# Kernel optimization log

Measured on AMD Instinct MI355X. Metric: run time of the kernel, lower is better.

## Reference

```python
import jax, jax.numpy as jnp
import numpy as np

GS, SO = 5, 3  # KANLinear grid_size, spline_order (efficient-kan defaults)


def kan_linear(x, base_w, spline_w, spline_scaler):
    """efficient-kan KANLinear: silu(x)@Wb^T + Bspline(x) contracted with scaled spline weights."""
    g = jnp.arange(-SO, GS + SO + 1, dtype=x.dtype) * (2.0 / GS) - 1.0  # uniform grid, len 12
    xe = x[..., None]                                                    # (..., in, 1)
    bases = ((xe >= g[:-1]) & (xe < g[1:])).astype(x.dtype)              # (..., in, 11)
    for k in range(1, SO + 1):  # Cox-de Boor recursion -> (..., in, 8)
        bases = ((xe - g[:-(k + 1)]) / (g[k:-1] - g[:-(k + 1)])) * bases[..., :-1] \
              + ((g[k + 1:] - xe) / (g[k + 1:] - g[1:-k])) * bases[..., 1:]
    out = jax.nn.silu(x) @ base_w.T
    return out + jnp.einsum('...ik,oik->...o', bases, spline_w * spline_scaler[..., None])


def reference(hidden_states, in_bw, in_sw, in_sc, conv_w, conv_b, x_bw, x_sw, x_sc,
              dt_w, dt_bias, A_logs, Ds, out_bw, out_sw, out_sc):
    B, N, L, Dm = hidden_states.shape
    d_inner, _, d_conv = conv_w.shape
    K = dt_bias.shape[0]          # 4 scan directions
    d_state = A_logs.shape[1]
    dt_rank = dt_w.shape[1]

    xz = kan_linear(hidden_states, in_bw, in_sw, in_sc)          # (B,N,L,2*Di)
    x, z = jnp.split(xz, 2, axis=-1)

    # causal depthwise conv1d + SiLU (torch pads both sides then truncates to L == left-pad)
    xc = x.reshape(B * N, L, d_inner).transpose(0, 2, 1)          # (BN,Di,L)
    xc = jax.lax.conv_general_dilated(xc, conv_w, (1,), [(d_conv - 1, 0)],
                                      dimension_numbers=('NCH', 'OIH', 'NCH'),
                                      feature_group_count=d_inner)
    xc = jax.nn.silu(xc + conv_b[None, :, None])
    x = xc.transpose(0, 2, 1).reshape(B, N, L, d_inner)

    xs = jnp.concatenate([x, jnp.flip(x, axis=2)], axis=1)        # (B,4,L,Di): fwd + seq-reversed

    x_dbl = kan_linear(xs, x_bw, x_sw, x_sc)                      # (B,4,L,R+2S)
    dt, Bs, Cs = jnp.split(x_dbl, [dt_rank, dt_rank + d_state], axis=-1)
    dts = dt @ dt_w.T                                             # (B,4,L,Di)
    delta = jax.nn.softplus(dts + dt_bias[None, :, None, :])      # (B,4,L,Di)
    A = -jnp.exp(A_logs).reshape(K, d_inner, d_state)             # (4,Di,S)

    # selective scan over L (serial data-dependent linear recurrence)
    u_t = xs.transpose(2, 0, 1, 3)      # (L,B,4,Di)
    d_t = delta.transpose(2, 0, 1, 3)   # (L,B,4,Di)
    B_t = Bs.transpose(2, 0, 1, 3)      # (L,B,4,S)
    C_t = Cs.transpose(2, 0, 1, 3)      # (L,B,4,S)

    def step(h, inp):
        u_l, dl, b_l, c_l = inp
        h = h * jnp.exp(dl[..., None] * A) + (dl * u_l)[..., None] * b_l[:, :, None, :]
        return h, jnp.einsum('bkdn,bkn->bkd', h, c_l)

    h0 = jnp.zeros((B, K, d_inner, d_state), xs.dtype)
    _, ys = jax.lax.scan(step, h0, (u_t, d_t, B_t, C_t))          # ys: (L,B,4,Di)

    y = ys.transpose(1, 2, 0, 3) + xs * Ds.reshape(K, d_inner)[None, :, None, :]  # (B,4,L,Di)
    y = y[:, :2] + jnp.flip(y[:, 2:4], axis=2)                    # merge forward/backward scans

    out = jnp.concatenate([y, z], axis=-1)                        # (B,2,L,2*Di)
    return kan_linear(out, out_bw, out_sw, out_sc)                # (B,2,L,Dm)


def setup_inputs() -> dict:
    key = jax.random.key(0)
    B, N, L = 2, 2, 1024
    d_model, d_state, d_conv, K = 512, 16, 4, 4
    d_inner = d_model            # expand=1
    dt_rank = 32                 # ceil(512/16)
    ks = jax.random.split(key, 10)

    def lin(k, o, i):
        return jax.random.normal(k, (o, i), jnp.float32) / np.sqrt(i).astype(np.float32)

    def spl(k, o, i):
        return jax.random.normal(k, (o, i, GS + SO), jnp.float32) * 0.05

    dt = jnp.exp(jax.random.uniform(ks[7], (d_inner,), jnp.float32)
                 * (np.log(0.1) - np.log(0.001)) + np.log(0.001))
    dt = jnp.clip(dt, 1e-4, None)
    inv_dt = dt + jnp.log(-jnp.expm1(-dt))

    std = dt_rank ** -0.5
    return {
        'hidden_states': jax.random.normal(ks[0], (B, N, L, d_model), jnp.float32),
        'in_bw': lin(ks[1], 2 * d_inner, d_model),
        'in_sw': spl(ks[2], 2 * d_inner, d_model),
        'in_sc': jnp.ones((2 * d_inner, d_model), jnp.float32),
        'conv_w': jax.random.normal(ks[3], (d_inner, 1, d_conv), jnp.float32) / np.sqrt(d_conv).astype(np.float32),
        'conv_b': jnp.zeros((d_inner,), jnp.float32),
        'x_bw': lin(ks[4], dt_rank + 2 * d_state, d_inner),
        'x_sw': spl(ks[5], dt_rank + 2 * d_state, d_inner),
        'x_sc': jnp.ones((dt_rank + 2 * d_state, d_inner), jnp.float32),
        'dt_w': jax.random.uniform(ks[6], (d_inner, dt_rank), jnp.float32, -std, std),
        'dt_bias': jnp.tile(inv_dt[None], (K, 1)),
        'A_logs': jnp.log(jnp.tile(jnp.arange(1, d_state + 1, dtype=jnp.float32)[None], (K * d_inner, 1))),
        'Ds': jnp.ones((K * d_inner,), jnp.float32),
        'out_bw': lin(ks[8], d_model, 2 * d_inner),
        'out_sw': spl(ks[9], d_model, 2 * d_inner),
        'out_sc': jnp.ones((d_model, 2 * d_inner), jnp.float32),
    }
```

## Files before the change

### kernel.cpp

```cpp
#include <hip/hip_runtime.h>
#include <stdint.h>

#define DEV __device__ __forceinline__

typedef __attribute__((ext_vector_type(8))) short short8;
typedef __attribute__((ext_vector_type(4))) float f32x4;

DEV unsigned short f2bf(float f) {
    union { float f; uint32_t u; } v; v.f = f;
    uint32_t u = v.u;
    return (unsigned short)((u + 0x7fffu + ((u >> 16) & 1u)) >> 16);
}
DEV float silu_f(float x) { return x / (1.0f + __expf(-x)); }

DEV void bspline8(float x, float* bo) {
    float b[11];
#pragma unroll
    for (int j = 0; j < 11; ++j) {
        float gj  = 0.4f * (float)(j - 3) - 1.0f;
        float gj1 = 0.4f * (float)(j - 2) - 1.0f;
        b[j] = (x >= gj && x < gj1) ? 1.0f : 0.0f;
    }
#pragma unroll
    for (int k = 1; k <= 3; ++k) {
        float inv = 1.0f / (0.4f * (float)k);
#pragma unroll
        for (int j = 0; j + k < 11; ++j) {
            float gj  = 0.4f * (float)(j - 3) - 1.0f;
            float gk1 = 0.4f * (float)(j + k - 2) - 1.0f;
            b[j] = ((x - gj) * b[j] + (gk1 - x) * b[j + 1]) * inv;
        }
    }
#pragma unroll
    for (int j = 0; j < 8; ++j) bo[j] = b[j];
}

__global__ __launch_bounds__(256) void zero_kernel(float4* __restrict__ p, int n4) {
    int i = blockIdx.x * 256 + threadIdx.x;
    if (i < n4) p[i] = make_float4(0.f, 0.f, 0.f, 0.f);
}

__global__ __launch_bounds__(256) void wc_kernel(const float* __restrict__ bw,
        const float* __restrict__ sw, const float* __restrict__ sc,
        unsigned short* __restrict__ Wc, int total) {
    int idx = blockIdx.x * 256 + threadIdx.x;
    if (idx >= total) return;
    float scale = sc[idx];
    unsigned short* o = Wc + (size_t)idx * 9;
    o[0] = f2bf(bw[idx]);
    const float* s = sw + (size_t)idx * 8;
#pragma unroll
    for (int j = 0; j < 8; ++j) o[1 + j] = f2bf(s[j] * scale);
}

__global__ __launch_bounds__(256) void feat_kernel(const float* __restrict__ X,
        unsigned short* __restrict__ F, int total) {
    int idx = blockIdx.x * 256 + threadIdx.x;
    if (idx >= total) return;
    float x = X[idx];
    unsigned short* o = F + (size_t)idx * 9;
    o[0] = f2bf(silu_f(x));
    float bo[8];
    bspline8(x, bo);
#pragma unroll
    for (int j = 0; j < 8; ++j) o[1 + j] = f2bf(bo[j]);
}

template<int BM, int BN, int DEPTH, bool ATOMIC>
__global__ __launch_bounds__(256) void gemm_mfma2(const unsigned short* __restrict__ A,
        const unsigned short* __restrict__ B, float* __restrict__ C,
        int M, int N, int K, int klen) {
    constexpr int NB  = DEPTH + 2;
    constexpr int FRM = BM / 32;
    constexpr int FRN = BN / 32;
    constexpr int GLA = (BM * 64) / 4096;
    constexpr int GLB = (BN * 64) / 4096;
    constexpr int GL  = GLA + GLB;
    constexpr int LDA = BM * 32;
    constexpr int LDB = BN * 32;
    __shared__ unsigned short As[NB * LDA];
    __shared__ unsigned short Bs[NB * LDB];

    const int tid = threadIdx.x;
    const int lane = tid & 63;
    const int w = tid >> 6;
    const int wr = w >> 1, wc = w & 1;
    const int bm = blockIdx.x * BM, bn = blockIdx.y * BN;
    const int kbase = blockIdx.z * klen;
    const int NT = klen / 32;
    const int frow = lane & 15;
    const int kq = (lane >> 4) * 8;

    f32x4 acc[FRM][FRN];
#pragma unroll
    for (int m = 0; m < FRM; ++m)
#pragma unroll
        for (int n = 0; n < FRN; ++n)
            acc[m][n] = (f32x4){0.f, 0.f, 0.f, 0.f};

    auto stage = [&](int t, int buf) {
        const int k0 = kbase + t * 32;
#pragma unroll
        for (int r = 0; r < GLA; ++r) {
            int bo = r * 4096 + tid * 16;
            int row = bo >> 6, cb = bo & 63;
            __builtin_amdgcn_global_load_lds(
                (const __attribute__((address_space(1))) void*)((const char*)A + ((size_t)(bm + row) * K + k0) * 2 + cb),
                (__attribute__((address_space(3))) void*)((char*)As + (size_t)buf * LDA * 2 + bo), 16, 0, 0);
        }
#pragma unroll
        for (int r = 0; r < GLB; ++r) {
            int bo = r * 4096 + tid * 16;
            int row = bo >> 6, cb = bo & 63;
            __builtin_amdgcn_global_load_lds(
                (const __attribute__((address_space(1))) void*)((const char*)B + ((size_t)(bn + row) * K + k0) * 2 + cb),
                (__attribute__((address_space(3))) void*)((char*)Bs + (size_t)buf * LDB * 2 + bo), 16, 0, 0);
        }
    };

    auto compute = [&](int buf) {
        const unsigned short* as = As + (size_t)buf * LDA;
        const unsigned short* bs = Bs + (size_t)buf * LDB;
        short8 af[FRM], bf[FRN];
#pragma unroll
        for (int m = 0; m < FRM; ++m)
            af[m] = *(const short8*)&as[(wr * (BM / 2) + m * 16 + frow) * 32 + kq];
#pragma unroll
        for (int n = 0; n < FRN; ++n)
            bf[n] = *(const short8*)&bs[(wc * (BN / 2) + n * 16 + frow) * 32 + kq];
#pragma unroll
        for (int m = 0; m < FRM; ++m)
#pragma unroll
            for (int n = 0; n < FRN; ++n)
                acc[m][n] = __builtin_amdgcn_mfma_f32_16x16x32_bf16(af[m], bf[n], acc[m][n], 0, 0, 0);
    };

    for (int t = 0; t < DEPTH; ++t) stage(t, t);

    int rb = 0;
    int sb = DEPTH;
    int t = 0;
    for (; t + DEPTH < NT; ++t) {
        stage(t + DEPTH, sb);
        asm volatile("s_waitcnt vmcnt(%0)" :: "i"(DEPTH * GL) : "memory");
        asm volatile("s_barrier" ::: "memory");
        compute(rb);
        rb = (rb + 1 == NB) ? 0 : rb + 1;
        sb = (sb + 1 == NB) ? 0 : sb + 1;
    }
    for (; t < NT; ++t) {
        asm volatile("s_waitcnt vmcnt(0)" ::: "memory");
        asm volatile("s_barrier" ::: "memory");
        compute(rb);
        rb = (rb + 1 == NB) ? 0 : rb + 1;
    }

    const int crow = (lane >> 4) * 4;
    const int ccol = lane & 15;
#pragma unroll
    for (int m = 0; m < FRM; ++m)
#pragma unroll
        for (int n = 0; n < FRN; ++n) {
            int gr = bm + wr * (BM / 2) + m * 16 + crow;
            int gc = bn + wc * (BN / 2) + n * 16 + ccol;
#pragma unroll
            for (int r = 0; r < 4; ++r) {
                if (ATOMIC) atomicAdd(&C[(size_t)(gr + r) * N + gc], acc[m][n][r]);
                else        C[(size_t)(gr + r) * N + gc] = acc[m][n][r];
            }
        }
}

__global__ __launch_bounds__(256) void conv_xs_kernel(const float* __restrict__ xz,
        const float* __restrict__ cw, const float* __restrict__ cb,
        float* __restrict__ xs) {
    int idx = blockIdx.x * 256 + threadIdx.x;
    int d = idx & 511;
    int l = (idx >> 9) & 1023;
    int bn = idx >> 19;
    const float* xcol = xz + (size_t)(bn * 1024) * 1024 + d;
    float acc = cb[d];
#pragma unroll
    for (int h = 0; h < 4; ++h) {
        int ls = l - 3 + h;
        float xv = (ls >= 0) ? xcol[(size_t)ls * 1024] : 0.0f;
        acc = fmaf(cw[d * 4 + h], xv, acc);
    }
    float v = silu_f(acc);
    int b = bn >> 1, nn = bn & 1;
    xs[((size_t)(b * 4 + nn) * 1024 + l) * 512 + d] = v;
    xs[((size_t)(b * 4 + nn + 2) * 1024 + (1023 - l)) * 512 + d] = v;
}

__global__ __launch_bounds__(256) void delta_kernel(const float* __restrict__ xdbl,
        const float* __restrict__ dtw, const float* __restrict__ dtb,
        float* __restrict__ delta) {
    int t = blockIdx.x >> 1;
    int half = blockIdx.x & 1;
    int d = half * 256 + threadIdx.x;
    __shared__ float dtv[32];
    if (threadIdx.x < 32) dtv[threadIdx.x] = xdbl[(size_t)t * 64 + threadIdx.x];
    __syncthreads();
    const float* w = dtw + (size_t)d * 32;
    float acc = 0.0f;
#pragma unroll
    for (int r = 0; r < 32; r += 4) {
        float4 wv = *(const float4*)(w + r);
        acc = fmaf(dtv[r], wv.x, acc);
        acc = fmaf(dtv[r + 1], wv.y, acc);
        acc = fmaf(dtv[r + 2], wv.z, acc);
        acc = fmaf(dtv[r + 3], wv.w, acc);
    }
    int k = (t >> 10) & 3;
    float x = acc + dtb[k * 512 + d];
    float sp = (x > 20.0f) ? x : log1pf(__expf(x));
    delta[(size_t)t * 512 + d] = sp;
}

__global__ __launch_bounds__(256) void scanA_kernel(const float* __restrict__ delta,
        const float* __restrict__ xs, const float* __restrict__ xdbl,
        const float* __restrict__ A_logs, float* __restrict__ P, float* __restrict__ Q) {
    int half = blockIdx.x & 1;
    int chunk = (blockIdx.x >> 1) & 15;
    int bk = blockIdx.x >> 5;
    int k = bk & 3;
    int d = half * 256 + threadIdx.x;
    __shared__ float Bl[64][16];
    for (int s = threadIdx.x; s < 64 * 16; s += 256) {
        int ll = s >> 4, n = s & 15;
        Bl[ll][n] = xdbl[(size_t)(bk * 1024 + chunk * 64 + ll) * 64 + 32 + n];
    }
    __syncthreads();
    float An[16];
#pragma unroll
    for (int n = 0; n < 16; ++n) An[n] = -__expf(A_logs[(size_t)(k * 512 + d) * 16 + n]);
    float h[16] = {};
    float p[16];
#pragma unroll
    for (int n = 0; n < 16; ++n) p[n] = 1.0f;
    int base = bk * 1024 + chunk * 64;
    for (int ll = 0; ll < 64; ++ll) {
        size_t off = (size_t)(base + ll) * 512 + d;
        float da = delta[off];
        float du = da * xs[off];
#pragma unroll
        for (int n = 0; n < 16; ++n) {
            float a = __expf(da * An[n]);
            h[n] = fmaf(h[n], a, du * Bl[ll][n]);
            p[n] *= a;
        }
    }
    size_t pb = ((size_t)(bk * 16 + chunk) * 16) * 512 + d;
#pragma unroll
    for (int n = 0; n < 16; ++n) { P[pb + n * 512] = p[n]; Q[pb + n * 512] = h[n]; }
}

__global__ __launch_bounds__(512) void scanB_kernel(const float* __restrict__ P,
        const float* __restrict__ Q, float* __restrict__ Hst) {
    int bk = blockIdx.x;
    int d = threadIdx.x;
    float h[16] = {};
    for (int chunk = 0; chunk < 16; ++chunk) {
        size_t base = ((size_t)(bk * 16 + chunk) * 16) * 512 + d;
#pragma unroll
        for (int n = 0; n < 16; ++n) {
            Hst[base + n * 512] = h[n];
            h[n] = fmaf(P[base + n * 512], h[n], Q[base + n * 512]);
        }
    }
}

__global__ __launch_bounds__(256) void scanC_kernel(const float* __restrict__ delta,
        float* __restrict__ xs, const float* __restrict__ xdbl,
        const float* __restrict__ A_logs, const float* __restrict__ Hst,
        const float* __restrict__ Ds) {
    int half = blockIdx.x & 1;
    int chunk = (blockIdx.x >> 1) & 15;
    int bk = blockIdx.x >> 5;
    int k = bk & 3;
    int d = half * 256 + threadIdx.x;
    __shared__ float BC[64][32];
    for (int s = threadIdx.x; s < 64 * 32; s += 256) {
        int ll = s >> 5, n = s & 31;
        BC[ll][n] = xdbl[(size_t)(bk * 1024 + chunk * 64 + ll) * 64 + 32 + n];
    }
    __syncthreads();
    float An[16];
#pragma unroll
    for (int n = 0; n < 16; ++n) An[n] = -__expf(A_logs[(size_t)(k * 512 + d) * 16 + n]);
    float h[16];
    size_t hb = ((size_t)(bk * 16 + chunk) * 16) * 512 + d;
#pragma unroll
    for (int n = 0; n < 16; ++n) h[n] = Hst[hb + n * 512];
    float Dv = Ds[k * 512 + d];
    int base = bk * 1024 + chunk * 64;
    for (int ll = 0; ll < 64; ++ll) {
        size_t off = (size_t)(base + ll) * 512 + d;
        float da = delta[off];
        float u = xs[off];
        float du = da * u;
        float y = 0.0f;
#pragma unroll
        for (int n = 0; n < 16; ++n) {
            float a = __expf(da * An[n]);
            h[n] = fmaf(h[n], a, du * BC[ll][n]);
            y = fmaf(h[n], BC[ll][16 + n], y);
        }
        xs[off] = fmaf(u, Dv, y);
    }
}

__global__ __launch_bounds__(256) void merge_kernel(const float* __restrict__ ys,
        float* __restrict__ xz) {
    int idx = blockIdx.x * 256 + threadIdx.x;
    int d = idx & 511;
    int l = (idx >> 9) & 1023;
    int nn = (idx >> 19) & 1;
    int b = idx >> 20;
    float v = ys[((size_t)(b * 4 + nn) * 1024 + l) * 512 + d]
            + ys[((size_t)(b * 4 + nn + 2) * 1024 + (1023 - l)) * 512 + d];
    size_t trow = (size_t)(b * 2 + nn) * 1024 + l;
    xz[trow * 1024 + d] = v;
}

extern "C" void kernel_launch(void* const* d_in, const int* in_sizes, int n_in,
                              void* d_out, int out_size, void* d_ws, size_t ws_size,
                              hipStream_t stream) {
    const float* hidden  = (const float*)d_in[0];
    const float* in_bw   = (const float*)d_in[1];
    const float* in_sw   = (const float*)d_in[2];
    const float* in_sc   = (const float*)d_in[3];
    const float* conv_w  = (const float*)d_in[4];
    const float* conv_b  = (const float*)d_in[5];
    const float* x_bw    = (const float*)d_in[6];
    const float* x_sw    = (const float*)d_in[7];
    const float* x_sc    = (const float*)d_in[8];
    const float* dt_w    = (const float*)d_in[9];
    const float* dt_bias = (const float*)d_in[10];
    const float* A_logs  = (const float*)d_in[11];
    const float* Ds      = (const float*)d_in[12];
    const float* out_bw  = (const float*)d_in[13];
    const float* out_sw  = (const float*)d_in[14];
    const float* out_sc  = (const float*)d_in[15];
    float* out = (float*)d_out;
    char* ws = (char*)d_ws;

    float* XZ    = (float*)(ws + 0);
    float* XS    = (float*)(ws + 16777216);
    float* XDBL  = (float*)(ws + 33554432);
    unsigned short* FEAT = (unsigned short*)(ws + 35651584);
    float* DELTA = (float*)(ws + 35651584);
    float* P     = (float*)(ws + 52428800);
    float* Q     = (float*)(ws + 56623104);
    float* HST   = (float*)(ws + 60817408);
    unsigned short* WCbuf = (unsigned short*)(ws + 111149056);
    unsigned short* WC2   = (unsigned short*)(ws + 120586240);

    wc_kernel<<<dim3((1024 * 512) / 256), 256, 0, stream>>>(in_bw, in_sw, in_sc, WCbuf, 1024 * 512);
    wc_kernel<<<dim3((64 * 512) / 256), 256, 0, stream>>>(x_bw, x_sw, x_sc, WC2, 64 * 512);

    feat_kernel<<<8192, 256, 0, stream>>>(hidden, FEAT, 4096 * 512);
    gemm_mfma2<128, 64, 3, false><<<dim3(32, 16, 1), 256, 0, stream>>>(FEAT, WCbuf, XZ, 4096, 1024, 4608, 4608);

    wc_kernel<<<dim3((512 * 1024) / 256), 256, 0, stream>>>(out_bw, out_sw, out_sc, WCbuf, 512 * 1024);

    conv_xs_kernel<<<8192, 256, 0, stream>>>(XZ, conv_w, conv_b, XS);

    feat_kernel<<<16384, 256, 0, stream>>>(XS, FEAT, 8192 * 512);
    zero_kernel<<<512, 256, 0, stream>>>((float4*)XDBL, (8192 * 64) / 4);
    gemm_mfma2<64, 64, 3, true><<<dim3(128, 1, 4), 256, 0, stream>>>(FEAT, WC2, XDBL, 8192, 64, 4608, 1152);

    delta_kernel<<<16384, 256, 0, stream>>>(XDBL, dt_w, dt_bias, DELTA);

    scanA_kernel<<<256, 256, 0, stream>>>(DELTA, XS, XDBL, A_logs, P, Q);
    scanB_kernel<<<8, 512, 0, stream>>>(P, Q, HST);
    scanC_kernel<<<256, 256, 0, stream>>>(DELTA, XS, XDBL, A_logs, HST, Ds);

    merge_kernel<<<8192, 256, 0, stream>>>(XS, XZ);

    feat_kernel<<<16384, 256, 0, stream>>>(XZ, FEAT, 4096 * 1024);
    zero_kernel<<<2048, 256, 0, stream>>>((float4*)out, (4096 * 512) / 4);
    gemm_mfma2<128, 64, 3, true><<<dim3(32, 8, 2), 256, 0, stream>>>(FEAT, WCbuf, out, 4096, 512, 9216, 4608);
}
```

Baseline: 524.6 us.

## Vectorize feature/weight packing, swizzle GEMM LDS, retile GEMMs with split-K

Feature and weight packing kernels now process 8 elements per thread and emit 16-byte vector stores in place of scattered 2-byte stores. The GEMM applies an XOR swizzle to the 16-byte chunks in LDS to reduce bank conflicts on fragment reads. The in-projection and out-projection GEMMs move to 128x128 tiles with split-K and atomic accumulation, which needs an extra zero pass over XZ. Atomic float accumulation changes summation order and adds atomic traffic.

```diff
diff --git a/kernel.cpp b/kernel.cpp
--- a/kernel.cpp
+++ b/kernel.cpp
@@ -40,30 +40,50 @@
     if (i < n4) p[i] = make_float4(0.f, 0.f, 0.f, 0.f);
 }
 
-__global__ __launch_bounds__(256) void wc_kernel(const float* __restrict__ bw,
+__global__ __launch_bounds__(256) void wc8_kernel(const float* __restrict__ bw,
         const float* __restrict__ sw, const float* __restrict__ sc,
         unsigned short* __restrict__ Wc, int total) {
-    int idx = blockIdx.x * 256 + threadIdx.x;
-    if (idx >= total) return;
-    float scale = sc[idx];
-    unsigned short* o = Wc + (size_t)idx * 9;
-    o[0] = f2bf(bw[idx]);
-    const float* s = sw + (size_t)idx * 8;
-#pragma unroll
-    for (int j = 0; j < 8; ++j) o[1 + j] = f2bf(s[j] * scale);
-}
-
-__global__ __launch_bounds__(256) void feat_kernel(const float* __restrict__ X,
+    int g = (blockIdx.x * 256 + threadIdx.x) * 8;
+    if (g >= total) return;
+    float bwv[8], scv[8], swv[64];
+    *(float4*)&bwv[0] = *(const float4*)&bw[g];
+    *(float4*)&bwv[4] = *(const float4*)&bw[g + 4];
+    *(float4*)&scv[0] = *(const float4*)&sc[g];
+    *(float4*)&scv[4] = *(const float4*)&sc[g + 4];
+#pragma unroll
+    for (int q = 0; q < 16; ++q) *(float4*)&swv[q * 4] = *(const float4*)&sw[(size_t)g * 8 + q * 4];
+    unsigned short buf[72];
+#pragma unroll
+    for (int e = 0; e < 8; ++e) {
+        buf[e * 9] = f2bf(bwv[e]);
+#pragma unroll
+        for (int j = 0; j < 8; ++j) buf[e * 9 + 1 + j] = f2bf(swv[e * 8 + j] * scv[e]);
+    }
+    unsigned short* o = Wc + (size_t)g * 9;
+#pragma unroll
+    for (int q = 0; q < 9; ++q) *(short8*)&o[q * 8] = *(short8*)&buf[q * 8];
+}
+
+__global__ __launch_bounds__(256) void feat8_kernel(const float* __restrict__ X,
         unsigned short* __restrict__ F, int total) {
-    int idx = blockIdx.x * 256 + threadIdx.x;
-    if (idx >= total) return;
-    float x = X[idx];
-    unsigned short* o = F + (size_t)idx * 9;
-    o[0] = f2bf(silu_f(x));
-    float bo[8];
-    bspline8(x, bo);
-#pragma unroll
-    for (int j = 0; j < 8; ++j) o[1 + j] = f2bf(bo[j]);
+    int g = (blockIdx.x * 256 + threadIdx.x) * 8;
+    if (g >= total) return;
+    float xv[8];
+    *(float4*)&xv[0] = *(const float4*)&X[g];
+    *(float4*)&xv[4] = *(const float4*)&X[g + 4];
+    unsigned short buf[72];
+#pragma unroll
+    for (int e = 0; e < 8; ++e) {
+        float x = xv[e];
+        buf[e * 9] = f2bf(silu_f(x));
+        float bo[8];
+        bspline8(x, bo);
+#pragma unroll
+        for (int j = 0; j < 8; ++j) buf[e * 9 + 1 + j] = f2bf(bo[j]);
+    }
+    unsigned short* o = F + (size_t)g * 9;
+#pragma unroll
+    for (int q = 0; q < 9; ++q) *(short8*)&o[q * 8] = *(short8*)&buf[q * 8];
 }
 
 template<int BM, int BN, int DEPTH, bool ATOMIC>
@@ -89,7 +109,7 @@
     const int kbase = blockIdx.z * klen;
     const int NT = klen / 32;
     const int frow = lane & 15;
-    const int kq = (lane >> 4) * 8;
+    const int uq = ((lane >> 4) ^ ((frow >> 1) & 3)) * 8;
 
     f32x4 acc[FRM][FRN];
 #pragma unroll
@@ -103,17 +123,19 @@
 #pragma unroll
         for (int r = 0; r < GLA; ++r) {
             int bo = r * 4096 + tid * 16;
-            int row = bo >> 6, cb = bo & 63;
+            int row = bo >> 6;
+            int lu = ((bo >> 4) & 3) ^ ((row >> 1) & 3);
             __builtin_amdgcn_global_load_lds(
-                (const __attribute__((address_space(1))) void*)((const char*)A + ((size_t)(bm + row) * K + k0) * 2 + cb),
+                (const __attribute__((address_space(1))) void*)((const char*)A + ((size_t)(bm + row) * K + k0) * 2 + lu * 16),
                 (__attribute__((address_space(3))) void*)((char*)As + (size_t)buf * LDA * 2 + bo), 16, 0, 0);
         }
 #pragma unroll
         for (int r = 0; r < GLB; ++r) {
             int bo = r * 4096 + tid * 16;
-            int row = bo >> 6, cb = bo & 63;
+            int row = bo >> 6;
+            int lu = ((bo >> 4) & 3) ^ ((row >> 1) & 3);
             __builtin_amdgcn_global_load_lds(
-                (const __attribute__((address_space(1))) void*)((const char*)B + ((size_t)(bn + row) * K + k0) * 2 + cb),
+                (const __attribute__((address_space(1))) void*)((const char*)B + ((size_t)(bn + row) * K + k0) * 2 + lu * 16),
                 (__attribute__((address_space(3))) void*)((char*)Bs + (size_t)buf * LDB * 2 + bo), 16, 0, 0);
         }
     };
@@ -124,10 +146,10 @@
         short8 af[FRM], bf[FRN];
 #pragma unroll
         for (int m = 0; m < FRM; ++m)
-            af[m] = *(const short8*)&as[(wr * (BM / 2) + m * 16 + frow) * 32 + kq];
+            af[m] = *(const short8*)&as[(wr * (BM / 2) + m * 16 + frow) * 32 + uq];
 #pragma unroll
         for (int n = 0; n < FRN; ++n)
-            bf[n] = *(const short8*)&bs[(wc * (BN / 2) + n * 16 + frow) * 32 + kq];
+            bf[n] = *(const short8*)&bs[(wc * (BN / 2) + n * 16 + frow) * 32 + uq];
 #pragma unroll
         for (int m = 0; m < FRM; ++m)
 #pragma unroll
@@ -356,17 +378,18 @@
     unsigned short* WCbuf = (unsigned short*)(ws + 111149056);
     unsigned short* WC2   = (unsigned short*)(ws + 120586240);
 
-    wc_kernel<<<dim3((1024 * 512) / 256), 256, 0, stream>>>(in_bw, in_sw, in_sc, WCbuf, 1024 * 512);
-    wc_kernel<<<dim3((64 * 512) / 256), 256, 0, stream>>>(x_bw, x_sw, x_sc, WC2, 64 * 512);
-
-    feat_kernel<<<8192, 256, 0, stream>>>(hidden, FEAT, 4096 * 512);
-    gemm_mfma2<128, 64, 3, false><<<dim3(32, 16, 1), 256, 0, stream>>>(FEAT, WCbuf, XZ, 4096, 1024, 4608, 4608);
-
-    wc_kernel<<<dim3((512 * 1024) / 256), 256, 0, stream>>>(out_bw, out_sw, out_sc, WCbuf, 512 * 1024);
+    wc8_kernel<<<256, 256, 0, stream>>>(in_bw, in_sw, in_sc, WCbuf, 1024 * 512);
+    wc8_kernel<<<16, 256, 0, stream>>>(x_bw, x_sw, x_sc, WC2, 64 * 512);
+
+    feat8_kernel<<<1024, 256, 0, stream>>>(hidden, FEAT, 4096 * 512);
+    zero_kernel<<<4096, 256, 0, stream>>>((float4*)XZ, (4096 * 1024) / 4);
+    gemm_mfma2<128, 128, 3, true><<<dim3(32, 8, 2), 256, 0, stream>>>(FEAT, WCbuf, XZ, 4096, 1024, 4608, 2304);
+
+    wc8_kernel<<<256, 256, 0, stream>>>(out_bw, out_sw, out_sc, WCbuf, 512 * 1024);
 
     conv_xs_kernel<<<8192, 256, 0, stream>>>(XZ, conv_w, conv_b, XS);
 
-    feat_kernel<<<16384, 256, 0, stream>>>(XS, FEAT, 8192 * 512);
+    feat8_kernel<<<2048, 256, 0, stream>>>(XS, FEAT, 8192 * 512);
     zero_kernel<<<512, 256, 0, stream>>>((float4*)XDBL, (8192 * 64) / 4);
     gemm_mfma2<64, 64, 3, true><<<dim3(128, 1, 4), 256, 0, stream>>>(FEAT, WC2, XDBL, 8192, 64, 4608, 1152);
 
@@ -378,7 +401,7 @@
 
     merge_kernel<<<8192, 256, 0, stream>>>(XS, XZ);
 
-    feat_kernel<<<16384, 256, 0, stream>>>(XZ, FEAT, 4096 * 1024);
+    feat8_kernel<<<2048, 256, 0, stream>>>(XZ, FEAT, 4096 * 1024);
     zero_kernel<<<2048, 256, 0, stream>>>((float4*)out, (4096 * 512) / 4);
-    gemm_mfma2<128, 64, 3, true><<<dim3(32, 8, 2), 256, 0, stream>>>(FEAT, WCbuf, out, 4096, 512, 9216, 4608);
-}
+    gemm_mfma2<128, 128, 3, true><<<dim3(32, 4, 4), 256, 0, stream>>>(FEAT, WCbuf, out, 4096, 512, 9216, 2304);
+}
```

Result: slower. 560.8 us (+6.9%).
